# Kernel optimization log

Hardware: AMD Instinct MI355X
Metric: run time of the kernel (lower is better)

The kernel has to match this reference:

```python
import jax, jax.numpy as jnp
import numpy as np

EPS = 1e-5

def _fake_quant(w, axis):
    # symmetric int8 fake-quant with straight-through estimator
    s = jnp.max(jnp.abs(w), axis=axis, keepdims=True) / 127.0 + 1e-8
    q = jnp.clip(jnp.round(w / s), -127.0, 127.0) * s
    return w + jax.lax.stop_gradient(q - w)

def _qconv1x1(x, w, b):
    # x: [B, C_in, Q, H, W]; w: [C_out, C_in] (1x1 kernel); weight fake-quantized
    wq = _fake_quant(w, axis=1)
    return jnp.einsum('bcqhw,oc->boqhw', x, wq) + b[None, :, None, None, None]

def setup_inputs() -> dict:
    key = jax.random.key(0)
    ks = jax.random.split(key, 12)
    B, C, Q, H, W = 8, 256, 4, 40, 40
    x = jax.random.normal(ks[0], (B, C, Q, H, W), dtype=jnp.float32)
    scale = 1.0 / np.sqrt(C)
    Wq = jax.random.normal(ks[1], (C, C), dtype=jnp.float32) * scale
    Wk = jax.random.normal(ks[2], (C, C), dtype=jnp.float32) * scale
    Wv = jax.random.normal(ks[3], (C, C), dtype=jnp.float32) * scale
    Wp = jax.random.normal(ks[4], (C, C), dtype=jnp.float32) * scale
    bq = jnp.zeros((C,), jnp.float32)
    bk = jnp.zeros((C,), jnp.float32)
    bv = jnp.zeros((C,), jnp.float32)
    bp = jnp.zeros((C,), jnp.float32)
    gamma = jnp.ones((C,), jnp.float32)
    beta = jnp.zeros((C,), jnp.float32)
    return {"x": x, "Wq": Wq, "bq": bq, "Wk": Wk, "bk": bk,
            "Wv": Wv, "bv": bv, "Wp": Wp, "bp": bp,
            "gamma": gamma, "beta": beta}

def reference(x, Wq, bq, Wk, bk, Wv, bv, Wp, bp, gamma, beta):
    B, C, Q, H, W = x.shape
    q = _qconv1x1(x, Wq, bq)
    k = _qconv1x1(x, Wk, bk)
    v = _qconv1x1(x, Wv, bv)
    # per-rotation channel attention: [B, Q=4, C, H*W]
    qh = q.reshape(B, C, Q, H * W).transpose(0, 2, 1, 3)
    kh = k.reshape(B, C, Q, H * W).transpose(0, 2, 1, 3)
    vh = v.reshape(B, C, Q, H * W).transpose(0, 2, 1, 3)
    scale = 1.0 / jnp.sqrt(jnp.float32(C // 4))
    attn = jnp.einsum('bqcn,bqdn->bqcd', qh, kh) * scale  # [B,4,C,C]
    attn = jax.nn.softmax(attn, axis=-1)
    out = jnp.einsum('bqcd,bqdn->bqcn', attn, vh)  # [B,4,C,HW]
    out = out.transpose(0, 2, 1, 3).reshape(B, C, Q, H, W)
    out = _qconv1x1(out, Wp, bp)
    # IQBN: per-channel batchnorm with int8 fake-quantized gamma
    mean = jnp.mean(out, axis=(0, 2, 3, 4), keepdims=True)
    var = jnp.var(out, axis=(0, 2, 3, 4), keepdims=True)
    g = _fake_quant(gamma, axis=None)[None, :, None, None, None]
    b = beta[None, :, None, None, None]
    out = (out - mean) * jax.lax.rsqrt(var + EPS) * g + b
    return out
```

## Files before the change

### kernel.cpp

```cpp
#include <hip/hip_runtime.h>
#include <math.h>

#define BB 8
#define CCH 256
#define QQ 4
#define NN 1600
#define BQN 32
#define SP 51200
#define EPSF 1e-5f

typedef __attribute__((ext_vector_type(8))) short bf16x8;
typedef __attribute__((ext_vector_type(4))) float f32x4;

static __device__ inline ushort f2bf(float f) {
  union { float f; unsigned u; } v; v.f = f;
  return (ushort)((v.u + 0x7fffu + ((v.u >> 16) & 1u)) >> 16);
}
static __device__ inline float bf2f(ushort u) {
  union { unsigned u; float f; } v; v.u = ((unsigned)u) << 16;
  return v.f;
}
static __device__ inline void gld16(const ushort* g, ushort* l) {
  __builtin_amdgcn_global_load_lds(
      (const __attribute__((address_space(1))) unsigned int*)g,
      (__attribute__((address_space(3))) unsigned int*)l, 16, 0, 0);
}

__global__ void quant_weights_kernel(const float* Wq, const float* Wk,
                                     const float* Wv, const float* Wp,
                                     const float* gamma,
                                     ushort* wq, ushort* wk, ushort* wvT, ushort* wp,
                                     ushort* wqT, ushort* wkT, ushort* wpT,
                                     float* gq, float* r, float* d2,
                                     float* m_acc, float* v_acc) {
  __shared__ float red[256];
  int blk = blockIdx.x;
  int tid = threadIdx.x;
  if (blk < 1024) {
    int mat = blk >> 8;
    int row = blk & 255;
    const float* W = (mat == 0) ? Wq : (mat == 1) ? Wk : (mat == 2) ? Wv : Wp;
    float w = W[row * 256 + tid];
    red[tid] = fabsf(w);
    __syncthreads();
    for (int s = 128; s > 0; s >>= 1) {
      if (tid < s) red[tid] = fmaxf(red[tid], red[tid + s]);
      __syncthreads();
    }
// ... 2 lines not shown
    ushort qb = f2bf(q);
    if (mat == 0)      { wq[row * 256 + tid] = qb; wqT[tid * 256 + row] = qb; }
    else if (mat == 1) { wk[row * 256 + tid] = qb; wkT[tid * 256 + row] = qb; }
    else if (mat == 2) { wvT[tid * 256 + row] = qb; }
    else               { wp[row * 256 + tid] = qb; wpT[tid * 256 + row] = qb; }
  } else {
    float g = gamma[tid];
    red[tid] = fabsf(g);
    __syncthreads();
    for (int s = 128; s > 0; s >>= 1) {
      if (tid < s) red[tid] = fmaxf(red[tid], red[tid + s]);
      __syncthreads();
    }
    float s = red[0] / 127.0f + 1e-8f;
    gq[tid] = fminf(fmaxf(rintf(g / s), -127.0f), 127.0f) * s;
    for (int i = tid; i < BQN * 256; i += 256) { r[i] = 0.f; d2[i] = 0.f; }
    m_acc[tid] = 0.f;
    v_acc[tid] = 0.f;
  }
}

__global__ __launch_bounds__(256)
void prep_kernel(const float* __restrict__ x, ushort* __restrict__ xb,
                 ushort* __restrict__ xT, float* __restrict__ r) {
  int bqi = blockIdx.z, b = bqi >> 2, q = bqi & 3;
  int s0 = blockIdx.x * 64, c0 = blockIdx.y * 64;
  __shared__ ushort lT[64 * 66];
  int tid = threadIdx.x;
  int c = tid >> 2, nch = (tid & 3) * 16;
  const float* xp = x + ((size_t)(b * CCH + c0 + c) * QQ + q) * NN + s0 + nch;
  union { ushort u[16]; int4 v[2]; } nb;
// ... 17 lines not shown
  *((int4*)xbp + 1) = nb.v[1];
  s += __shfl_down(s, 2);
  s += __shfl_down(s, 1);
  if ((tid & 3) == 0) atomicAdd(&r[bqi * 256 + c0 + c], s);
  __syncthreads();
  int n = tid >> 2, cch = (tid & 3) * 16;
  union { ushort u[16]; int4 v[2]; } o;
#pragma unroll
  for (int i = 0; i < 16; i++) o.u[i] = lT[(cch + i) * 66 + n];
  ushort* dst = xT + (size_t)(bqi * NN + s0 + n) * CCH + c0 + cch;
  *(int4*)dst = o.v[0];
  *((int4*)dst + 1) = o.v[1];
}

__global__ __launch_bounds__(256)
void gram_sym_kernel(const ushort* __restrict__ xb, ushort* __restrict__ Gh,
                     ushort* __restrict__ Gl) {
  __shared__ __align__(16) char smem[16384];
  int t = blockIdx.x, z = blockIdx.y;
  int ty = (t >= 4) + (t >= 7) + (t >= 9);
  int base = ty * 4 - (ty * (ty - 1)) / 2;
  int tx = ty + (t - base);
  int mBase = ty * 64, nBase = tx * 64;
  bool offd = (tx != ty);
  int tid = threadIdx.x, wave = tid >> 6, lane = tid & 63;
  int wm = wave >> 1, wn = wave & 1;
  int col = lane & 15, quad = lane >> 4;
  const ushort* X = xb + (size_t)z * (CCH * NN);
  const ushort* gA = X + (size_t)(mBase + (tid >> 2)) * NN + (tid & 3) * 8;
  const ushort* gB = X + (size_t)(nBase + (tid >> 2)) * NN + (tid & 3) * 8;
  f32x4 acc[2][2];
#pragma unroll
  for (int i = 0; i < 2; i++)
#pragma unroll
    for (int j = 0; j < 2; j++) acc[i][j] = (f32x4){0.f, 0.f, 0.f, 0.f};

  const int nIter = NN / 32;
  gld16(gA, (ushort*)smem + tid * 8);
  gld16(gB, (ushort*)(smem + 4096) + tid * 8);
  for (int it = 0; it < nIter; ++it) {
    int cur = it & 1;
    __syncthreads();
    if (it + 1 < nIter) {
      int kt = (it + 1) << 5;
      char* bb = smem + (cur ^ 1) * 8192;
      gld16(gA + kt, (ushort*)bb + tid * 8);
      gld16(gB + kt, (ushort*)(bb + 4096) + tid * 8);
    }
    const ushort* lA = (const ushort*)(smem + cur * 8192);
    const ushort* lB = lA + 2048;
    bf16x8 af[2], bfr[2];
#pragma unroll
    for (int i = 0; i < 2; i++)
      af[i] = *(const bf16x8*)&lA[(wm * 32 + i * 16 + col) * 32 + quad * 8];
#pragma unroll
    for (int j = 0; j < 2; j++)
      bfr[j] = *(const bf16x8*)&lB[(wn * 32 + j * 16 + col) * 32 + quad * 8];
#pragma unroll
    for (int i = 0; i < 2; i++)
#pragma unroll
      for (int j = 0; j < 2; j++)
        acc[i][j] = __builtin_amdgcn_mfma_f32_16x16x32_bf16(af[i], bfr[j], acc[i][j], 0, 0, 0);
  }
  __syncthreads();
  float* lCw = (float*)smem + wave * 576;
#pragma unroll
  for (int i = 0; i < 2; i++) {
#pragma unroll
    for (int j = 0; j < 2; j++)
#pragma unroll
      for (int rg = 0; rg < 4; rg++)
        lCw[(quad * 4 + rg) * 36 + j * 16 + col] = acc[i][j][rg];
    int mrow0 = mBase + wm * 32 + i * 16;
    int nW = nBase + wn * 32;
    int rr = lane >> 2, cc = (lane & 3) * 8;
    union { ushort u[8]; int4 v; } oh, ol;
#pragma unroll
    for (int t8 = 0; t8 < 8; t8++) {
      float vfl = lCw[rr * 36 + cc + t8];
      ushort hh = f2bf(vfl);
// ... 8 lines not shown
      union { ushort u[8]; int4 v; } th, tl;
#pragma unroll
      for (int t8 = 0; t8 < 8; t8++) {
        float vfl = lCw[(mh + t8) * 36 + nn];
        ushort hh = f2bf(vfl);
        th.u[t8] = hh;
        tl.u[t8] = f2bf(vfl - bf2f(hh));
      }
      size_t offT = (size_t)z * 65536 + (size_t)(nW + nn) * 256 + mrow0 + mh;
      *(int4*)(Gh + offT) = th.v;
      *(int4*)(Gl + offT) = tl.v;
    }
  }
}

__global__ __launch_bounds__(256)
void spk_kernel(const ushort* __restrict__ wq, const ushort* __restrict__ Gh,
                const ushort* __restrict__ Gl, const ushort* __restrict__ wk,
                const float* __restrict__ ug, const float* __restrict__ vg,
                const float* __restrict__ bqv, const float* __restrict__ bkv,
                const float* __restrict__ bvv,
                ushort* __restrict__ P, float* __restrict__ pb) {
  __shared__ __align__(16) char smem[103424];
  int z = blockIdx.y, mBase = blockIdx.x * 32;
  int tid = threadIdx.x, wave = tid >> 6, lane = tid & 63;
  int col = lane & 15, quad = lane >> 4;
  int rA = tid >> 2, sub = (tid & 3) * 8;
  const ushort* Ghz = Gh + (size_t)z * 65536;
  const ushort* Glz = Gl + (size_t)z * 65536;
  ushort* M1h_l = (ushort*)(smem + 69632);
  ushort* M1l_l = M1h_l + 8448;

  f32x4 acc[2][4];
#pragma unroll
  for (int i = 0; i < 2; i++)
#pragma unroll
    for (int j = 0; j < 4; j++) acc[i][j] = (f32x4){0.f, 0.f, 0.f, 0.f};

  auto s1_load = [&](int buf, int kt) {
    ushort* L = (ushort*)(smem + buf * 34816);
    if (tid < 128)
      gld16(wq + (size_t)(mBase + rA) * 256 + kt + sub, L + tid * 8);
    ushort* Lh = L + 1024;
    ushort* Ll = L + 9216;
#pragma unroll
    for (int q = 0; q < 4; q++) {
      int n = q * 64 + rA;
      gld16(Ghz + (size_t)n * 256 + kt + sub, Lh + (q * 256 + tid) * 8);
      gld16(Glz + (size_t)n * 256 + kt + sub, Ll + (q * 256 + tid) * 8);
    }
  };
  s1_load(0, 0);
  for (int it = 0; it < 8; ++it) {
    int cur = it & 1;
    __syncthreads();
    if (it + 1 < 8) s1_load(cur ^ 1, (it + 1) * 32);
    const ushort* L = (const ushort*)(smem + cur * 34816);
    const ushort* lA = L;
    const ushort* lBh = L + 1024;
    const ushort* lBl = L + 9216;
    bf16x8 af[2], bh[4], bl[4];
#pragma unroll
    for (int i = 0; i < 2; i++)
      af[i] = *(const bf16x8*)&lA[(i * 16 + col) * 32 + quad * 8];
#pragma unroll
    for (int j = 0; j < 4; j++) {
      bh[j] = *(const bf16x8*)&lBh[(wave * 64 + j * 16 + col) * 32 + quad * 8];
      bl[j] = *(const bf16x8*)&lBl[(wave * 64 + j * 16 + col) * 32 + quad * 8];
    }
#pragma unroll
    for (int i = 0; i < 2; i++)
#pragma unroll
      for (int j = 0; j < 4; j++) {
        acc[i][j] = __builtin_amdgcn_mfma_f32_16x16x32_bf16(af[i], bh[j], acc[i][j], 0, 0, 0);
        acc[i][j] = __builtin_amdgcn_mfma_f32_16x16x32_bf16(af[i], bl[j], acc[i][j], 0, 0, 0);
      }
  }
#pragma unroll
  for (int i = 0; i < 2; i++)
#pragma unroll
    for (int j = 0; j < 4; j++)
#pragma unroll
      for (int rg = 0; rg < 4; rg++) {
        int ml = i * 16 + quad * 4 + rg;
        int cg = wave * 64 + j * 16 + col;
        float vfl = acc[i][j][rg];
        ushort hh = f2bf(vfl);
        M1h_l[ml * 264 + cg] = hh;
        M1l_l[ml * 264 + cg] = f2bf(vfl - bf2f(hh));
      }

  f32x4 acc2[2][4];
#pragma unroll
  for (int i = 0; i < 2; i++)
#pragma unroll
    for (int j = 0; j < 4; j++) acc2[i][j] = (f32x4){0.f, 0.f, 0.f, 0.f};
  auto s2_load = [&](int buf, int kt) {
    ushort* L = (ushort*)(smem + buf * 34816);
#pragma unroll
    for (int q = 0; q < 4; q++)
      gld16(wk + (size_t)(q * 64 + rA) * 256 + kt + sub, L + (q * 256 + tid) * 8);
  };
  s2_load(0, 0);
  for (int it = 0; it < 8; ++it) {
    int cur = it & 1;
    __syncthreads();
    if (it + 1 < 8) s2_load(cur ^ 1, (it + 1) * 32);
    const ushort* lB = (const ushort*)(smem + cur * 34816);
    int kt = it * 32;
    bf16x8 ah[2], al[2], bfr[4];
#pragma unroll
    for (int i = 0; i < 2; i++) {
      ah[i] = *(const bf16x8*)&M1h_l[(i * 16 + col) * 264 + kt + quad * 8];
      al[i] = *(const bf16x8*)&M1l_l[(i * 16 + col) * 264 + kt + quad * 8];
    }
#pragma unroll
    for (int j = 0; j < 4; j++)
      bfr[j] = *(const bf16x8*)&lB[(wave * 64 + j * 16 + col) * 32 + quad * 8];
#pragma unroll
    for (int i = 0; i < 2; i++)
#pragma unroll
      for (int j = 0; j < 4; j++) {
        acc2[i][j] = __builtin_amdgcn_mfma_f32_16x16x32_bf16(ah[i], bfr[j], acc2[i][j], 0, 0, 0);
        acc2[i][j] = __builtin_amdgcn_mfma_f32_16x16x32_bf16(al[i], bfr[j], acc2[i][j], 0, 0, 0);
      }
  }
  __syncthreads();

  float* Sb = (float*)(smem + 69632);
  float bkc[4], vvc[4];
#pragma unroll
  for (int j = 0; j < 4; j++) {
    int cg = wave * 64 + j * 16 + col;
    bkc[j] = bkv[cg];
    vvc[j] = vg[z * 256 + cg];
  }
#pragma unroll
  for (int i = 0; i < 2; i++)
#pragma unroll
    for (int rg = 0; rg < 4; rg++) {
      int ml = i * 16 + quad * 4 + rg;
      int rglob = mBase + ml;
      float uu = ug[z * 256 + rglob];
      float bqc = bqv[rglob];
#pragma unroll
      for (int j = 0; j < 4; j++)
        Sb[ml * 260 + wave * 64 + j * 16 + col] =
            0.125f * (acc2[i][j][rg] + uu * bkc[j] + bqc * vvc[j] + 1600.0f * bqc * bkc[j]);
    }
  __syncthreads();

  float4 bv4 = *(const float4*)(bvv + lane * 4);
#pragma unroll
  for (int rr8 = 0; rr8 < 8; ++rr8) {
    int rloc = wave * 8 + rr8;
    f32x4 sv = *(const f32x4*)&Sb[rloc * 260 + lane * 4];
    float x0 = sv[0], x1 = sv[1], x2 = sv[2], x3 = sv[3];
    float m = fmaxf(fmaxf(x0, x1), fmaxf(x2, x3));
#pragma unroll
    for (int s = 32; s > 0; s >>= 1) m = fmaxf(m, __shfl_xor(m, s));
    float e0 = expf(x0 - m), e1 = expf(x1 - m), e2 = expf(x2 - m), e3 = expf(x3 - m);
    float t = e0 + e1 + e2 + e3;
#pragma unroll
    for (int s = 32; s > 0; s >>= 1) t += __shfl_xor(t, s);
    float is = 1.0f / t;
    float p0 = e0 * is, p1 = e1 * is, p2 = e2 * is, p3 = e3 * is;
    union { ushort u[4]; uint2 v; } o;
    o.u[0] = f2bf(p0); o.u[1] = f2bf(p1); o.u[2] = f2bf(p2); o.u[3] = f2bf(p3);
    *(uint2*)(P + (size_t)z * 65536 + (size_t)(mBase + rloc) * 256 + lane * 4) = o.v;
    float d = p0 * bv4.x + p1 * bv4.y + p2 * bv4.z + p3 * bv4.w;
#pragma unroll
    for (int s = 32; s > 0; s >>= 1) d += __shfl_xor(d, s);
    if (lane == 0) pb[z * 256 + mBase + rloc] = d;
  }
}

__global__ __launch_bounds__(256)
void pt_kernel(const ushort* __restrict__ P, const ushort* __restrict__ wvT,
               const ushort* __restrict__ wp,
               ushort* __restrict__ Tm, ushort* __restrict__ TmT) {
  __shared__ __align__(16) char smem[53760];
  int z = blockIdx.y, cs = blockIdx.x * 32;
  int tid = threadIdx.x, wave = tid >> 6, lane = tid & 63;
  int col = lane & 15, quad = lane >> 4;
  int rA = tid >> 2, sub = (tid & 3) * 8;
  const ushort* Pz = P + (size_t)z * 65536;
  ushort* N1b = (ushort*)(smem + 36864);

  f32x4 acc[4][2];
#pragma unroll
  for (int i = 0; i < 4; i++)
#pragma unroll
    for (int j = 0; j < 2; j++) acc[i][j] = (f32x4){0.f, 0.f, 0.f, 0.f};
  auto s3_load = [&](int buf, int kt) {
    ushort* L = (ushort*)(smem + buf * 18432);
#pragma unroll
    for (int q = 0; q < 4; q++)
      gld16(Pz + (size_t)(q * 64 + rA) * 256 + kt + sub, L + (q * 256 + tid) * 8);
    if (tid < 128)
      gld16(wvT + (size_t)(cs + rA) * 256 + kt + sub, L + 8192 + tid * 8);
  };
  s3_load(0, 0);
  for (int it = 0; it < 8; ++it) {
    int cur = it & 1;
    __syncthreads();
    if (it + 1 < 8) s3_load(cur ^ 1, (it + 1) * 32);
    const ushort* lP = (const ushort*)(smem + cur * 18432);
    const ushort* lV = lP + 8192;
    bf16x8 af[4], bfr[2];
#pragma unroll
    for (int i = 0; i < 4; i++)
      af[i] = *(const bf16x8*)&lP[(wave * 64 + i * 16 + col) * 32 + quad * 8];
#pragma unroll
    for (int j = 0; j < 2; j++)
      bfr[j] = *(const bf16x8*)&lV[(j * 16 + col) * 32 + quad * 8];
#pragma unroll
    for (int i = 0; i < 4; i++)
#pragma unroll
      for (int j = 0; j < 2; j++)
        acc[i][j] = __builtin_amdgcn_mfma_f32_16x16x32_bf16(af[i], bfr[j], acc[i][j], 0, 0, 0);
  }
#pragma unroll
  for (int i = 0; i < 4; i++)
#pragma unroll
    for (int j = 0; j < 2; j++)
#pragma unroll
      for (int rg = 0; rg < 4; rg++) {
        int e = wave * 64 + i * 16 + quad * 4 + rg;
        int cl = j * 16 + col;
        N1b[cl * 264 + e] = f2bf(acc[i][j][rg]);
      }

  f32x4 acc2[4][2];
#pragma unroll
  for (int i = 0; i < 4; i++)
#pragma unroll
    for (int j = 0; j < 2; j++) acc2[i][j] = (f32x4){0.f, 0.f, 0.f, 0.f};
  auto s4_load = [&](int buf, int kt) {
    ushort* L = (ushort*)(smem + buf * 18432);
#pragma unroll
    for (int q = 0; q < 4; q++)
      gld16(wp + (size_t)(q * 64 + rA) * 256 + kt + sub, L + (q * 256 + tid) * 8);
  };
  s4_load(0, 0);
  for (int it = 0; it < 8; ++it) {
    int cur = it & 1;
    __syncthreads();
    if (it + 1 < 8) s4_load(cur ^ 1, (it + 1) * 32);
    const ushort* lW = (const ushort*)(smem + cur * 18432);
    int kt = it * 32;
    bf16x8 af[4], bfr[2];
#pragma unroll
    for (int i = 0; i < 4; i++)
      af[i] = *(const bf16x8*)&lW[(wave * 64 + i * 16 + col) * 32 + quad * 8];
#pragma unroll
    for (int j = 0; j < 2; j++)
      bfr[j] = *(const bf16x8*)&N1b[(j * 16 + col) * 264 + kt + quad * 8];
#pragma unroll
    for (int i = 0; i < 4; i++)
#pragma unroll
      for (int j = 0; j < 2; j++)
        acc2[i][j] = __builtin_amdgcn_mfma_f32_16x16x32_bf16(af[i], bfr[j], acc2[i][j], 0, 0, 0);
  }
  __syncthreads();
  float* lCw = (float*)smem + wave * 576;
#pragma unroll
  for (int i = 0; i < 4; i++) {
#pragma unroll
    for (int j = 0; j < 2; j++)
#pragma unroll
      for (int rg = 0; rg < 4; rg++)
        lCw[(quad * 4 + rg) * 36 + j * 16 + col] = acc2[i][j][rg];
    int oW = wave * 64 + i * 16;
    int rr = lane >> 2, cc = (lane & 3) * 8;
    union { ushort u[8]; int4 v; } o;
#pragma unroll
    for (int t8 = 0; t8 < 8; t8++) o.u[t8] = f2bf(lCw[rr * 36 + cc + t8]);
    *(int4*)(Tm + (size_t)z * 65536 + (size_t)(oW + rr) * 256 + cs + cc) = o.v;
    int nn = lane >> 1, mh = (lane & 1) * 8;
    union { ushort u[8]; int4 v; } o2;
#pragma unroll
    for (int t8 = 0; t8 < 8; t8++) o2.u[t8] = f2bf(lCw[(mh + t8) * 36 + nn]);
    *(int4*)(TmT + (size_t)z * 65536 + (size_t)(cs + nn) * 256 + oW + mh) = o2.v;
  }
}

template<int MODE>
__global__ __launch_bounds__(256)
void gemm64(const ushort* __restrict__ A, long sA, const ushort* __restrict__ A2,
            const ushort* __restrict__ B, long sB, const ushort* __restrict__ B2,
            void* __restrict__ C1, void* __restrict__ C2, long sC) {
  constexpr bool SPB = (MODE == 0 || MODE == 4);
  constexpr bool SPA = (MODE == 1);
  constexpr int BUFB = (SPA || SPB) ? 12288 : 8192;
  __shared__ __align__(16) char smem[2 * BUFB];
  int z = blockIdx.z;
  int mBase = blockIdx.y * 64, nBase = blockIdx.x * 64;
  int tid = threadIdx.x, wave = tid >> 6, lane = tid & 63;
  int wm = wave >> 1, wn = wave & 1;
  int col = lane & 15, quad = lane >> 4;
  const ushort* gA = A + (size_t)z * sA + (size_t)(mBase + (tid >> 2)) * 256 + (tid & 3) * 8;
  const ushort* gB = B + (size_t)z * sB + (size_t)(nBase + (tid >> 2)) * 256 + (tid & 3) * 8;
  const ushort* gX = nullptr;
  if (SPB) gX = B2 + (size_t)z * sB + (size_t)(nBase + (tid >> 2)) * 256 + (tid & 3) * 8;
  if (SPA) gX = A2 + (size_t)z * sA + (size_t)(mBase + (tid >> 2)) * 256 + (tid & 3) * 8;

  f32x4 acc[2][2];
#pragma unroll
  for (int i = 0; i < 2; i++)
#pragma unroll
    for (int j = 0; j < 2; j++) acc[i][j] = (f32x4){0.f, 0.f, 0.f, 0.f};

  {
    char* bb = smem;
    gld16(gA, (ushort*)bb + tid * 8);
    gld16(gB, (ushort*)(bb + 4096) + tid * 8);
    if (SPA || SPB) gld16(gX, (ushort*)(bb + 8192) + tid * 8);
  }
  for (int it = 0; it < 8; ++it) {
    int cur = it & 1;
    __syncthreads();
    if (it + 1 < 8) {
      int kt = (it + 1) * 32;
      char* bb = smem + (cur ^ 1) * BUFB;
      gld16(gA + kt, (ushort*)bb + tid * 8);
      gld16(gB + kt, (ushort*)(bb + 4096) + tid * 8);
      if (SPA || SPB) gld16(gX + kt, (ushort*)(bb + 8192) + tid * 8);
    }
    const ushort* lA = (const ushort*)(smem + cur * BUFB);
    const ushort* lB = lA + 2048;
    const ushort* lX = lA + 4096;
    bf16x8 af[2], bfv[2], xf[2];
#pragma unroll
    for (int i = 0; i < 2; i++)
      af[i] = *(const bf16x8*)&lA[(wm * 32 + i * 16 + col) * 32 + quad * 8];
#pragma unroll
    for (int j = 0; j < 2; j++)
      bfv[j] = *(const bf16x8*)&lB[(wn * 32 + j * 16 + col) * 32 + quad * 8];
    if (SPB) {
#pragma unroll
      for (int j = 0; j < 2; j++)
        xf[j] = *(const bf16x8*)&lX[(wn * 32 + j * 16 + col) * 32 + quad * 8];
    } else if (SPA) {
#pragma unroll
      for (int i = 0; i < 2; i++)
        xf[i] = *(const bf16x8*)&lX[(wm * 32 + i * 16 + col) * 32 + quad * 8];
    }
#pragma unroll
    for (int i = 0; i < 2; i++)
#pragma unroll
      for (int j = 0; j < 2; j++) {
        acc[i][j] = __builtin_amdgcn_mfma_f32_16x16x32_bf16(af[i], bfv[j], acc[i][j], 0, 0, 0);
        if (SPB)
          acc[i][j] = __builtin_amdgcn_mfma_f32_16x16x32_bf16(af[i], xf[j], acc[i][j], 0, 0, 0);
        if (SPA)
          acc[i][j] = __builtin_amdgcn_mfma_f32_16x16x32_bf16(xf[i], bfv[j], acc[i][j], 0, 0, 0);
      }
  }

  if (MODE == 4) {
    const ushort* Tz = A + (size_t)z * sA;
    float* d2 = (float*)C1;
#pragma unroll
    for (int i = 0; i < 2; i++) {
      int mr = mBase + wm * 32 + i * 16 + quad * 4;
#pragma unroll
      for (int rg = 0; rg < 4; rg++) {
        float p = 0.f;
#pragma unroll
        for (int j = 0; j < 2; j++)
          p += acc[i][j][rg] * bf2f(Tz[(mr + rg) * 256 + nBase + wn * 32 + j * 16 + col]);
        p += __shfl_down(p, 8);
        p += __shfl_down(p, 4);
        p += __shfl_down(p, 2);
        p += __shfl_down(p, 1);
        if (col == 0) atomicAdd(d2 + z * 256 + mr + rg, p);
      }
    }
    return;
  }
}

__global__ __launch_bounds__(256)
void uv_kernel(const ushort* __restrict__ wqT, const ushort* __restrict__ wkT,
               const float* __restrict__ r, float* __restrict__ u,
               float* __restrict__ vv) {
  int bq = blockIdx.x, sel = blockIdx.y, c = threadIdx.x;
  __shared__ float rs[256];
  rs[c] = r[bq * 256 + c];
  __syncthreads();
  const ushort* WT = sel ? wkT : wqT;
  float s = 0.f;
  for (int i = 0; i < 256; i++) s += bf2f(WT[i * 256 + c]) * rs[i];
  (sel ? vv : u)[bq * 256 + c] = s;
}

__global__ __launch_bounds__(256)
void bo_d1_kernel(const ushort* __restrict__ wpT, const ushort* __restrict__ TmT,
                  const float* __restrict__ pb, const float* __restrict__ rb,
                  const float* __restrict__ bp, const float* __restrict__ d2,
                  float* __restrict__ bo, float* __restrict__ m_acc,
                  float* __restrict__ v_acc) {
  int z = blockIdx.x, o = threadIdx.x;
  __shared__ float sp[256], sr[256];
  sp[o] = pb[z * 256 + o];
  sr[o] = rb[z * 256 + o];
  __syncthreads();
  float bv = bp[o], d1 = 0.f;
  const ushort* Tz = TmT + (size_t)z * 65536;
  for (int c = 0; c < 256; c++) {
    bv += bf2f(wpT[c * 256 + o]) * sp[c];
    d1 += bf2f(Tz[c * 256 + o]) * sr[c];
  }
  bo[z * 256 + o] = bv;
  atomicAdd(m_acc + o, d1 + 1600.0f * bv);
  atomicAdd(v_acc + o, d2[z * 256 + o] + 2.0f * bv * d1 + 1600.0f * bv * bv);
}

__global__ __launch_bounds__(256)
void final_kernel(const ushort* __restrict__ Tm, const ushort* __restrict__ xT,
                  const float* __restrict__ bo, const float* __restrict__ m_acc,
                  const float* __restrict__ v_acc, const float* __restrict__ gq,
                  const float* __restrict__ beta, float* __restrict__ out) {
  __shared__ __align__(16) char smem[32768];
  float* lC = (float*)smem;
  int z = blockIdx.z;
  int mBase = blockIdx.y * 128, nBase = blockIdx.x * 128;
  int tid = threadIdx.x, wave = tid >> 6, lane = tid & 63;
  int wm = wave >> 1, wn = wave & 1;
  int col = lane & 15, quad = lane >> 4;
  int srow = tid >> 2, skc = (tid & 3) * 8;
// ... 107 lines not shown
  ushort* wqT  = wvT + 65536;
  ushort* wkT  = wqT + 65536;
  ushort* wpT  = wkT + 65536;
  ushort* xb   = wpT + 65536;
  ushort* xT   = xb + (size_t)BQN * CCH * NN;
  ushort* Gh   = xT + (size_t)BQN * CCH * NN;
  ushort* Gl   = Gh + (size_t)BQN * 65536;
  ushort* P    = Gl + (size_t)BQN * 65536;
  ushort* Tm   = P + (size_t)BQN * 65536;
  ushort* TmT  = Tm + (size_t)BQN * 65536;
  float*  r    = (float*)(TmT + (size_t)BQN * 65536);
  float*  u    = r + 8192;
  float*  vv   = u + 8192;
  float*  pb   = vv + 8192;
  float*  bo   = pb + 8192;
  float*  d2   = bo + 8192;
  float*  m_acc = d2 + 8192;
  float*  v_acc = m_acc + 256;
  float*  gq   = v_acc + 256;

  quant_weights_kernel<<<1025, 256, 0, stream>>>(Wq, Wk, Wv, Wp, gamma,
                                                 wq, wk, wvT, wp, wqT, wkT, wpT,
                                                 gq, r, d2, m_acc, v_acc);
  prep_kernel<<<dim3(NN / 64, CCH / 64, BQN), 256, 0, stream>>>(x, xb, xT, r);
  uv_kernel<<<dim3(BQN, 2), 256, 0, stream>>>(wqT, wkT, r, u, vv);
  gram_sym_kernel<<<dim3(10, BQN), 256, 0, stream>>>(xb, Gh, Gl);
  spk_kernel<<<dim3(8, BQN), 256, 0, stream>>>(wq, Gh, Gl, wk, u, vv, bq, bk, bv, P, pb);
  pt_kernel<<<dim3(8, BQN), 256, 0, stream>>>(P, wvT, wp, Tm, TmT);
  gemm64<4><<<dim3(4, 4, BQN), 256, 0, stream>>>(
      Tm, 65536, nullptr, Gh, 65536, Gl, d2, nullptr, 0);
  bo_d1_kernel<<<BQN, 256, 0, stream>>>(wpT, TmT, pb, r, bp, d2, bo, m_acc, v_acc);
  final_kernel<<<dim3(13, 2, BQN), 256, 0, stream>>>(Tm, xT, bo, m_acc, v_acc,
                                                     gq, beta, out);
}
```

Before: 250.9 us.

## Load MFMA operands directly from global, fuse uv into gram, widen spk/pt blocks

Replaces LDS double-buffered global_load_lds staging in the gram, spk, pt and d2 GEMMs with direct per-lane 16-byte global loads feeding MFMA. It folds the uv reduction into an extra block of the gram kernel and moves spk and pt to 512-thread blocks with smaller per-wave tiles and less shared memory. The d2 buffer is dropped and its values are accumulated straight into v_acc. This saves launches, LDS traffic and barriers, but relies on L1/L2 for operand reuse and loses explicit load/compute overlap.

```diff
diff --git a/kernel.cpp b/kernel.cpp
--- a/kernel.cpp
+++ b/kernel.cpp
@@ -20,6 +20,9 @@
   union { unsigned u; float f; } v; v.u = ((unsigned)u) << 16;
   return v.f;
 }
+static __device__ inline bf16x8 ldg8(const ushort* p) {
+  return *(const bf16x8*)p;
+}
 static __device__ inline void gld16(const ushort* g, ushort* l) {
   __builtin_amdgcn_global_load_lds(
       (const __attribute__((address_space(1))) unsigned int*)g,
@@ -31,7 +34,7 @@
                                      const float* gamma,
                                      ushort* wq, ushort* wk, ushort* wvT, ushort* wp,
                                      ushort* wqT, ushort* wkT, ushort* wpT,
-                                     float* gq, float* r, float* d2,
+                                     float* gq, float* r,
                                      float* m_acc, float* v_acc) {
   __shared__ float red[256];
   int blk = blockIdx.x;
@@ -64,7 +67,7 @@
     }
     float s = red[0] / 127.0f + 1e-8f;
     gq[tid] = fminf(fmaxf(rintf(g / s), -127.0f), 127.0f) * s;
-    for (int i = tid; i < BQN * 256; i += 256) { r[i] = 0.f; d2[i] = 0.f; }
+    for (int i = tid; i < BQN * 256; i += 256) r[i] = 0.f;
     m_acc[tid] = 0.f;
     v_acc[tid] = 0.f;
   }
@@ -112,56 +115,56 @@
 }
 
 __global__ __launch_bounds__(256)
-void gram_sym_kernel(const ushort* __restrict__ xb, ushort* __restrict__ Gh,
-                     ushort* __restrict__ Gl) {
-  __shared__ __align__(16) char smem[16384];
+void gram_uv_kernel(const ushort* __restrict__ xb, ushort* __restrict__ Gh,
+                    ushort* __restrict__ Gl,
+                    const ushort* __restrict__ wqT, const ushort* __restrict__ wkT,
+                    const float* __restrict__ r, float* __restrict__ u,
+                    float* __restrict__ vv) {
+  __shared__ __align__(16) float lCw_s[2304];
+  __shared__ float rs[256];
   int t = blockIdx.x, z = blockIdx.y;
+  int tid = threadIdx.x;
+  if (t == 10) {
+    rs[tid] = r[z * 256 + tid];
+    __syncthreads();
+    float su = 0.f, sv = 0.f;
+    for (int i = 0; i < 256; i++) {
+      float rv = rs[i];
+      su += bf2f(wqT[i * 256 + tid]) * rv;
+      sv += bf2f(wkT[i * 256 + tid]) * rv;
+    }
+    u[z * 256 + tid] = su;
+    vv[z * 256 + tid] = sv;
+    return;
+  }
   int ty = (t >= 4) + (t >= 7) + (t >= 9);
   int base = ty * 4 - (ty * (ty - 1)) / 2;
   int tx = ty + (t - base);
   int mBase = ty * 64, nBase = tx * 64;
   bool offd = (tx != ty);
-  int tid = threadIdx.x, wave = tid >> 6, lane = tid & 63;
+  int wave = tid >> 6, lane = tid & 63;
   int wm = wave >> 1, wn = wave & 1;
   int col = lane & 15, quad = lane >> 4;
   const ushort* X = xb + (size_t)z * (CCH * NN);
-  const ushort* gA = X + (size_t)(mBase + (tid >> 2)) * NN + (tid & 3) * 8;
-  const ushort* gB = X + (size_t)(nBase + (tid >> 2)) * NN + (tid & 3) * 8;
+  const ushort* pA0 = X + (size_t)(mBase + wm * 32 + col) * NN + quad * 8;
+  const ushort* pA1 = pA0 + (size_t)16 * NN;
+  const ushort* pB0 = X + (size_t)(nBase + wn * 32 + col) * NN + quad * 8;
+  const ushort* pB1 = pB0 + (size_t)16 * NN;
   f32x4 acc[2][2];
 #pragma unroll
   for (int i = 0; i < 2; i++)
 #pragma unroll
     for (int j = 0; j < 2; j++) acc[i][j] = (f32x4){0.f, 0.f, 0.f, 0.f};
-
-  const int nIter = NN / 32;
-  gld16(gA, (ushort*)smem + tid * 8);
-  gld16(gB, (ushort*)(smem + 4096) + tid * 8);
-  for (int it = 0; it < nIter; ++it) {
-    int cur = it & 1;
-    __syncthreads();
-    if (it + 1 < nIter) {
-      int kt = (it + 1) << 5;
-      char* bb = smem + (cur ^ 1) * 8192;
-      gld16(gA + kt, (ushort*)bb + tid * 8);
-      gld16(gB + kt, (ushort*)(bb + 4096) + tid * 8);
-    }
-    const ushort* lA = (const ushort*)(smem + cur * 8192);
-    const ushort* lB = lA + 2048;
-    bf16x8 af[2], bfr[2];
-#pragma unroll
-    for (int i = 0; i < 2; i++)
-      af[i] = *(const bf16x8*)&lA[(wm * 32 + i * 16 + col) * 32 + quad * 8];
-#pragma unroll
-    for (int j = 0; j < 2; j++)
-      bfr[j] = *(const bf16x8*)&lB[(wn * 32 + j * 16 + col) * 32 + quad * 8];
-#pragma unroll
-    for (int i = 0; i < 2; i++)
-#pragma unroll
-      for (int j = 0; j < 2; j++)
-        acc[i][j] = __builtin_amdgcn_mfma_f32_16x16x32_bf16(af[i], bfr[j], acc[i][j], 0, 0, 0);
-  }
-  __syncthreads();
-  float* lCw = (float*)smem + wave * 576;
+#pragma unroll 2
+  for (int kk = 0; kk < NN; kk += 32) {
+    bf16x8 a0 = ldg8(pA0 + kk), a1 = ldg8(pA1 + kk);
+    bf16x8 b0 = ldg8(pB0 + kk), b1 = ldg8(pB1 + kk);
+    acc[0][0] = __builtin_amdgcn_mfma_f32_16x16x32_bf16(a0, b0, acc[0][0], 0, 0, 0);
+    acc[0][1] = __builtin_amdgcn_mfma_f32_16x16x32_bf16(a0, b1, acc[0][1], 0, 0, 0);
+    acc[1][0] = __builtin_amdgcn_mfma_f32_16x16x32_bf16(a1, b0, acc[1][0], 0, 0, 0);
+    acc[1][1] = __builtin_amdgcn_mfma_f32_16x16x32_bf16(a1, b1, acc[1][1], 0, 0, 0);
+  }
+  float* lCw = lCw_s + wave * 576;
 #pragma unroll
   for (int i = 0; i < 2; i++) {
 #pragma unroll
@@ -200,124 +203,96 @@
   }
 }
 
-__global__ __launch_bounds__(256)
+__global__ __launch_bounds__(512)
 void spk_kernel(const ushort* __restrict__ wq, const ushort* __restrict__ Gh,
                 const ushort* __restrict__ Gl, const ushort* __restrict__ wk,
                 const float* __restrict__ ug, const float* __restrict__ vg,
                 const float* __restrict__ bqv, const float* __restrict__ bkv,
                 const float* __restrict__ bvv,
                 ushort* __restrict__ P, float* __restrict__ pb) {
-  __shared__ __align__(16) char smem[103424];
+  __shared__ __align__(16) char smem[33792];
+  ushort* M1h_l = (ushort*)smem;
+  ushort* M1l_l = M1h_l + 8448;
   int z = blockIdx.y, mBase = blockIdx.x * 32;
-  int tid = threadIdx.x, wave = tid >> 6, lane = tid & 63;
+  int tid = threadIdx.x, w = tid >> 6, lane = tid & 63;
   int col = lane & 15, quad = lane >> 4;
-  int rA = tid >> 2, sub = (tid & 3) * 8;
   const ushort* Ghz = Gh + (size_t)z * 65536;
   const ushort* Glz = Gl + (size_t)z * 65536;
-  ushort* M1h_l = (ushort*)(smem + 69632);
-  ushort* M1l_l = M1h_l + 8448;
-
-  f32x4 acc[2][4];
-#pragma unroll
-  for (int i = 0; i < 2; i++)
-#pragma unroll
-    for (int j = 0; j < 4; j++) acc[i][j] = (f32x4){0.f, 0.f, 0.f, 0.f};
-
-  auto s1_load = [&](int buf, int kt) {
-    ushort* L = (ushort*)(smem + buf * 34816);
-    if (tid < 128)
-      gld16(wq + (size_t)(mBase + rA) * 256 + kt + sub, L + tid * 8);
-    ushort* Lh = L + 1024;
-    ushort* Ll = L + 9216;
-#pragma unroll
-    for (int q = 0; q < 4; q++) {
-      int n = q * 64 + rA;
-      gld16(Ghz + (size_t)n * 256 + kt + sub, Lh + (q * 256 + tid) * 8);
-      gld16(Glz + (size_t)n * 256 + kt + sub, Ll + (q * 256 + tid) * 8);
-    }
-  };
-  s1_load(0, 0);
-  for (int it = 0; it < 8; ++it) {
-    int cur = it & 1;
-    __syncthreads();
-    if (it + 1 < 8) s1_load(cur ^ 1, (it + 1) * 32);
-    const ushort* L = (const ushort*)(smem + cur * 34816);
-    const ushort* lA = L;
-    const ushort* lBh = L + 1024;
-    const ushort* lBl = L + 9216;
-    bf16x8 af[2], bh[4], bl[4];
-#pragma unroll
-    for (int i = 0; i < 2; i++)
-      af[i] = *(const bf16x8*)&lA[(i * 16 + col) * 32 + quad * 8];
-#pragma unroll
-    for (int j = 0; j < 4; j++) {
-      bh[j] = *(const bf16x8*)&lBh[(wave * 64 + j * 16 + col) * 32 + quad * 8];
-      bl[j] = *(const bf16x8*)&lBl[(wave * 64 + j * 16 + col) * 32 + quad * 8];
-    }
-#pragma unroll
-    for (int i = 0; i < 2; i++)
-#pragma unroll
-      for (int j = 0; j < 4; j++) {
-        acc[i][j] = __builtin_amdgcn_mfma_f32_16x16x32_bf16(af[i], bh[j], acc[i][j], 0, 0, 0);
-        acc[i][j] = __builtin_amdgcn_mfma_f32_16x16x32_bf16(af[i], bl[j], acc[i][j], 0, 0, 0);
-      }
-  }
-#pragma unroll
-  for (int i = 0; i < 2; i++)
-#pragma unroll
-    for (int j = 0; j < 4; j++)
+
+  f32x4 acc[2][2];
+#pragma unroll
+  for (int i = 0; i < 2; i++)
+#pragma unroll
+    for (int j = 0; j < 2; j++) acc[i][j] = (f32x4){0.f, 0.f, 0.f, 0.f};
+  {
+    const ushort* pA0 = wq + (size_t)(mBase + col) * 256 + quad * 8;
+    const ushort* pA1 = pA0 + 16 * 256;
+    const ushort* pH0 = Ghz + (size_t)(w * 32 + col) * 256 + quad * 8;
+    const ushort* pH1 = pH0 + 16 * 256;
+    const ushort* pL0 = Glz + (size_t)(w * 32 + col) * 256 + quad * 8;
+    const ushort* pL1 = pL0 + 16 * 256;
+#pragma unroll
+    for (int kk = 0; kk < 256; kk += 32) {
+      bf16x8 a0 = ldg8(pA0 + kk), a1 = ldg8(pA1 + kk);
+      bf16x8 h0 = ldg8(pH0 + kk), h1 = ldg8(pH1 + kk);
+      bf16x8 l0 = ldg8(pL0 + kk), l1 = ldg8(pL1 + kk);
+      acc[0][0] = __builtin_amdgcn_mfma_f32_16x16x32_bf16(a0, h0, acc[0][0], 0, 0, 0);
+      acc[0][0] = __builtin_amdgcn_mfma_f32_16x16x32_bf16(a0, l0, acc[0][0], 0, 0, 0);
+      acc[0][1] = __builtin_amdgcn_mfma_f32_16x16x32_bf16(a0, h1, acc[0][1], 0, 0, 0);
+      acc[0][1] = __builtin_amdgcn_mfma_f32_16x16x32_bf16(a0, l1, acc[0][1], 0, 0, 0);
+      acc[1][0] = __builtin_amdgcn_mfma_f32_16x16x32_bf16(a1, h0, acc[1][0], 0, 0, 0);
+      acc[1][0] = __builtin_amdgcn_mfma_f32_16x16x32_bf16(a1, l0, acc[1][0], 0, 0, 0);
+      acc[1][1] = __builtin_amdgcn_mfma_f32_16x16x32_bf16(a1, h1, acc[1][1], 0, 0, 0);
+      acc[1][1] = __builtin_amdgcn_mfma_f32_16x16x32_bf16(a1, l1, acc[1][1], 0, 0, 0);
+    }
+  }
+#pragma unroll
+  for (int i = 0; i < 2; i++)
+#pragma unroll
+    for (int j = 0; j < 2; j++)
 #pragma unroll
       for (int rg = 0; rg < 4; rg++) {
         int ml = i * 16 + quad * 4 + rg;
-        int cg = wave * 64 + j * 16 + col;
+        int cg = w * 32 + j * 16 + col;
         float vfl = acc[i][j][rg];
         ushort hh = f2bf(vfl);
         M1h_l[ml * 264 + cg] = hh;
         M1l_l[ml * 264 + cg] = f2bf(vfl - bf2f(hh));
       }
-
-  f32x4 acc2[2][4];
-#pragma unroll
-  for (int i = 0; i < 2; i++)
-#pragma unroll
-    for (int j = 0; j < 4; j++) acc2[i][j] = (f32x4){0.f, 0.f, 0.f, 0.f};
-  auto s2_load = [&](int buf, int kt) {
-    ushort* L = (ushort*)(smem + buf * 34816);
-#pragma unroll
-    for (int q = 0; q < 4; q++)
-      gld16(wk + (size_t)(q * 64 + rA) * 256 + kt + sub, L + (q * 256 + tid) * 8);
-  };
-  s2_load(0, 0);
-  for (int it = 0; it < 8; ++it) {
-    int cur = it & 1;
-    __syncthreads();
-    if (it + 1 < 8) s2_load(cur ^ 1, (it + 1) * 32);
-    const ushort* lB = (const ushort*)(smem + cur * 34816);
-    int kt = it * 32;
-    bf16x8 ah[2], al[2], bfr[4];
-#pragma unroll
-    for (int i = 0; i < 2; i++) {
-      ah[i] = *(const bf16x8*)&M1h_l[(i * 16 + col) * 264 + kt + quad * 8];
-      al[i] = *(const bf16x8*)&M1l_l[(i * 16 + col) * 264 + kt + quad * 8];
-    }
-#pragma unroll
-    for (int j = 0; j < 4; j++)
-      bfr[j] = *(const bf16x8*)&lB[(wave * 64 + j * 16 + col) * 32 + quad * 8];
-#pragma unroll
-    for (int i = 0; i < 2; i++)
-#pragma unroll
-      for (int j = 0; j < 4; j++) {
-        acc2[i][j] = __builtin_amdgcn_mfma_f32_16x16x32_bf16(ah[i], bfr[j], acc2[i][j], 0, 0, 0);
-        acc2[i][j] = __builtin_amdgcn_mfma_f32_16x16x32_bf16(al[i], bfr[j], acc2[i][j], 0, 0, 0);
-      }
-  }
-  __syncthreads();
-
-  float* Sb = (float*)(smem + 69632);
-  float bkc[4], vvc[4];
-#pragma unroll
-  for (int j = 0; j < 4; j++) {
-    int cg = wave * 64 + j * 16 + col;
+  __syncthreads();
+
+  f32x4 acc2[2][2];
+#pragma unroll
+  for (int i = 0; i < 2; i++)
+#pragma unroll
+    for (int j = 0; j < 2; j++) acc2[i][j] = (f32x4){0.f, 0.f, 0.f, 0.f};
+  {
+    const ushort* pW0 = wk + (size_t)(w * 32 + col) * 256 + quad * 8;
+    const ushort* pW1 = pW0 + 16 * 256;
+#pragma unroll
+    for (int kk = 0; kk < 256; kk += 32) {
+      bf16x8 ah0 = *(const bf16x8*)&M1h_l[(col) * 264 + kk + quad * 8];
+      bf16x8 ah1 = *(const bf16x8*)&M1h_l[(16 + col) * 264 + kk + quad * 8];
+      bf16x8 al0 = *(const bf16x8*)&M1l_l[(col) * 264 + kk + quad * 8];
+      bf16x8 al1 = *(const bf16x8*)&M1l_l[(16 + col) * 264 + kk + quad * 8];
+      bf16x8 b0 = ldg8(pW0 + kk), b1 = ldg8(pW1 + kk);
+      acc2[0][0] = __builtin_amdgcn_mfma_f32_16x16x32_bf16(ah0, b0, acc2[0][0], 0, 0, 0);
+      acc2[0][0] = __builtin_amdgcn_mfma_f32_16x16x32_bf16(al0, b0, acc2[0][0], 0, 0, 0);
+      acc2[0][1] = __builtin_amdgcn_mfma_f32_16x16x32_bf16(ah0, b1, acc2[0][1], 0, 0, 0);
+      acc2[0][1] = __builtin_amdgcn_mfma_f32_16x16x32_bf16(al0, b1, acc2[0][1], 0, 0, 0);
+      acc2[1][0] = __builtin_amdgcn_mfma_f32_16x16x32_bf16(ah1, b0, acc2[1][0], 0, 0, 0);
+      acc2[1][0] = __builtin_amdgcn_mfma_f32_16x16x32_bf16(al1, b0, acc2[1][0], 0, 0, 0);
+      acc2[1][1] = __builtin_amdgcn_mfma_f32_16x16x32_bf16(ah1, b1, acc2[1][1], 0, 0, 0);
+      acc2[1][1] = __builtin_amdgcn_mfma_f32_16x16x32_bf16(al1, b1, acc2[1][1], 0, 0, 0);
+    }
+  }
+  __syncthreads();
+
+  float* Sb = (float*)smem;
+  float bkc[2], vvc[2];
+#pragma unroll
+  for (int j = 0; j < 2; j++) {
+    int cg = w * 32 + j * 16 + col;
     bkc[j] = bkv[cg];
     vvc[j] = vg[z * 256 + cg];
   }
@@ -330,16 +305,16 @@
       float uu = ug[z * 256 + rglob];
       float bqc = bqv[rglob];
 #pragma unroll
-      for (int j = 0; j < 4; j++)
-        Sb[ml * 260 + wave * 64 + j * 16 + col] =
+      for (int j = 0; j < 2; j++)
+        Sb[ml * 260 + w * 32 + j * 16 + col] =
             0.125f * (acc2[i][j][rg] + uu * bkc[j] + bqc * vvc[j] + 1600.0f * bqc * bkc[j]);
     }
   __syncthreads();
 
   float4 bv4 = *(const float4*)(bvv + lane * 4);
 #pragma unroll
-  for (int rr8 = 0; rr8 < 8; ++rr8) {
-    int rloc = wave * 8 + rr8;
+  for (int rr4 = 0; rr4 < 4; ++rr4) {
+    int rloc = w * 4 + rr4;
     f32x4 sv = *(const f32x4*)&Sb[rloc * 260 + lane * 4];
     float x0 = sv[0], x1 = sv[1], x2 = sv[2], x3 = sv[3];
     float m = fmaxf(fmaxf(x0, x1), fmaxf(x2, x3));
@@ -361,103 +336,79 @@
   }
 }
 
-__global__ __launch_bounds__(256)
+__global__ __launch_bounds__(512)
 void pt_kernel(const ushort* __restrict__ P, const ushort* __restrict__ wvT,
                const ushort* __restrict__ wp,
                ushort* __restrict__ Tm, ushort* __restrict__ TmT) {
-  __shared__ __align__(16) char smem[53760];
+  __shared__ __align__(16) char smem[18432];
+  ushort* N1b = (ushort*)smem;
   int z = blockIdx.y, cs = blockIdx.x * 32;
-  int tid = threadIdx.x, wave = tid >> 6, lane = tid & 63;
+  int tid = threadIdx.x, w = tid >> 6, lane = tid & 63;
   int col = lane & 15, quad = lane >> 4;
-  int rA = tid >> 2, sub = (tid & 3) * 8;
   const ushort* Pz = P + (size_t)z * 65536;
-  ushort* N1b = (ushort*)(smem + 36864);
-
-  f32x4 acc[4][2];
-#pragma unroll
-  for (int i = 0; i < 4; i++)
+
+  f32x4 acc[2][2];
+#pragma unroll
+  for (int i = 0; i < 2; i++)
 #pragma unroll
     for (int j = 0; j < 2; j++) acc[i][j] = (f32x4){0.f, 0.f, 0.f, 0.f};
-  auto s3_load = [&](int buf, int kt) {
-    ushort* L = (ushort*)(smem + buf * 18432);
-#pragma unroll
-    for (int q = 0; q < 4; q++)
-      gld16(Pz + (size_t)(q * 64 + rA) * 256 + kt + sub, L + (q * 256 + tid) * 8);
-    if (tid < 128)
-      gld16(wvT + (size_t)(cs + rA) * 256 + kt + sub, L + 8192 + tid * 8);
-  };
-  s3_load(0, 0);
-  for (int it = 0; it < 8; ++it) {
-    int cur = it & 1;
-    __syncthreads();
-    if (it + 1 < 8) s3_load(cur ^ 1, (it + 1) * 32);
-    const ushort* lP = (const ushort*)(smem + cur * 18432);
-    const ushort* lV = lP + 8192;
-    bf16x8 af[4], bfr[2];
-#pragma unroll
-    for (int i = 0; i < 4; i++)
-      af[i] = *(const bf16x8*)&lP[(wave * 64 + i * 16 + col) * 32 + quad * 8];
+  {
+    const ushort* pP0 = Pz + (size_t)(w * 32 + col) * 256 + quad * 8;
+    const ushort* pP1 = pP0 + 16 * 256;
+    const ushort* pV0 = wvT + (size_t)(cs + col) * 256 + quad * 8;
+    const ushort* pV1 = pV0 + 16 * 256;
+#pragma unroll
+    for (int kk = 0; kk < 256; kk += 32) {
+      bf16x8 a0 = ldg8(pP0 + kk), a1 = ldg8(pP1 + kk);
+      bf16x8 b0 = ldg8(pV0 + kk), b1 = ldg8(pV1 + kk);
+      acc[0][0] = __builtin_amdgcn_mfma_f32_16x16x32_bf16(a0, b0, acc[0][0], 0, 0, 0);
+      acc[0][1] = __builtin_amdgcn_mfma_f32_16x16x32_bf16(a0, b1, acc[0][1], 0, 0, 0);
+      acc[1][0] = __builtin_amdgcn_mfma_f32_16x16x32_bf16(a1, b0, acc[1][0], 0, 0, 0);
+      acc[1][1] = __builtin_amdgcn_mfma_f32_16x16x32_bf16(a1, b1, acc[1][1], 0, 0, 0);
+    }
+  }
+#pragma unroll
+  for (int i = 0; i < 2; i++)
 #pragma unroll
     for (int j = 0; j < 2; j++)
-      bfr[j] = *(const bf16x8*)&lV[(j * 16 + col) * 32 + quad * 8];
-#pragma unroll
-    for (int i = 0; i < 4; i++)
-#pragma unroll
-      for (int j = 0; j < 2; j++)
-        acc[i][j] = __builtin_amdgcn_mfma_f32_16x16x32_bf16(af[i], bfr[j], acc[i][j], 0, 0, 0);
-  }
-#pragma unroll
-  for (int i = 0; i < 4; i++)
-#pragma unroll
-    for (int j = 0; j < 2; j++)
 #pragma unroll
       for (int rg = 0; rg < 4; rg++) {
-        int e = wave * 64 + i * 16 + quad * 4 + rg;
+        int e = w * 32 + i * 16 + quad * 4 + rg;
         int cl = j * 16 + col;
         N1b[cl * 264 + e] = f2bf(acc[i][j][rg]);
       }
-
-  f32x4 acc2[4][2];
-#pragma unroll
-  for (int i = 0; i < 4; i++)
+  __syncthreads();
+
+  f32x4 acc2[2][2];
+#pragma unroll
+  for (int i = 0; i < 2; i++)
 #pragma unroll
     for (int j = 0; j < 2; j++) acc2[i][j] = (f32x4){0.f, 0.f, 0.f, 0.f};
-  auto s4_load = [&](int buf, int kt) {
-    ushort* L = (ushort*)(smem + buf * 18432);
-#pragma unroll
-    for (int q = 0; q < 4; q++)
-      gld16(wp + (size_t)(q * 64 + rA) * 256 + kt + sub, L + (q * 256 + tid) * 8);
-  };
-  s4_load(0, 0);
-  for (int it = 0; it < 8; ++it) {
-    int cur = it & 1;
-    __syncthreads();
-    if (it + 1 < 8) s4_load(cur ^ 1, (it + 1) * 32);
-    const ushort* lW = (const ushort*)(smem + cur * 18432);
-    int kt = it * 32;
-    bf16x8 af[4], bfr[2];
-#pragma unroll
-    for (int i = 0; i < 4; i++)
-      af[i] = *(const bf16x8*)&lW[(wave * 64 + i * 16 + col) * 32 + quad * 8];
-#pragma unroll
-    for (int j = 0; j < 2; j++)
-      bfr[j] = *(const bf16x8*)&N1b[(j * 16 + col) * 264 + kt + quad * 8];
-#pragma unroll
-    for (int i = 0; i < 4; i++)
-#pragma unroll
-      for (int j = 0; j < 2; j++)
-        acc2[i][j] = __builtin_amdgcn_mfma_f32_16x16x32_bf16(af[i], bfr[j], acc2[i][j], 0, 0, 0);
-  }
-  __syncthreads();
-  float* lCw = (float*)smem + wave * 576;
-#pragma unroll
-  for (int i = 0; i < 4; i++) {
+  {
+    const ushort* pW0 = wp + (size_t)(w * 32 + col) * 256 + quad * 8;
+    const ushort* pW1 = pW0 + 16 * 256;
+#pragma unroll
+    for (int kk = 0; kk < 256; kk += 32) {
+      bf16x8 a0 = ldg8(pW0 + kk), a1 = ldg8(pW1 + kk);
+      bf16x8 b0 = *(const bf16x8*)&N1b[(col) * 264 + kk + quad * 8];
+      bf16x8 b1 = *(const bf16x8*)&N1b[(16 + col) * 264 + kk + quad * 8];
+      acc2[0][0] = __builtin_amdgcn_mfma_f32_16x16x32_bf16(a0, b0, acc2[0][0], 0, 0, 0);
+      acc2[0][1] = __builtin_amdgcn_mfma_f32_16x16x32_bf16(a0, b1, acc2[0][1], 0, 0, 0);
+      acc2[1][0] = __builtin_amdgcn_mfma_f32_16x16x32_bf16(a1, b0, acc2[1][0], 0, 0, 0);
+      acc2[1][1] = __builtin_amdgcn_mfma_f32_16x16x32_bf16(a1, b1, acc2[1][1], 0, 0, 0);
+    }
+  }
+  __syncthreads();
+
+  float* lCw = (float*)smem + w * 576;
+#pragma unroll
+  for (int i = 0; i < 2; i++) {
 #pragma unroll
     for (int j = 0; j < 2; j++)
 #pragma unroll
       for (int rg = 0; rg < 4; rg++)
         lCw[(quad * 4 + rg) * 36 + j * 16 + col] = acc2[i][j][rg];
-    int oW = wave * 64 + i * 16;
+    int oW = w * 32 + i * 16;
     int rr = lane >> 2, cc = (lane & 3) * 8;
     union { ushort u[8]; int4 v; } o;
 #pragma unroll
@@ -471,120 +422,64 @@
   }
 }
 
-template<int MODE>
 __global__ __launch_bounds__(256)
-void gemm64(const ushort* __restrict__ A, long sA, const ushort* __restrict__ A2,
-            const ushort* __restrict__ B, long sB, const ushort* __restrict__ B2,
-            void* __restrict__ C1, void* __restrict__ C2, long sC) {
-  constexpr bool SPB = (MODE == 0 || MODE == 4);
-  constexpr bool SPA = (MODE == 1);
-  constexpr int BUFB = (SPA || SPB) ? 12288 : 8192;
-  __shared__ __align__(16) char smem[2 * BUFB];
+void dsq_kernel(const ushort* __restrict__ Tm, const ushort* __restrict__ Gh,
+                const ushort* __restrict__ Gl, float* __restrict__ v_acc) {
   int z = blockIdx.z;
   int mBase = blockIdx.y * 64, nBase = blockIdx.x * 64;
   int tid = threadIdx.x, wave = tid >> 6, lane = tid & 63;
   int wm = wave >> 1, wn = wave & 1;
   int col = lane & 15, quad = lane >> 4;
-  const ushort* gA = A + (size_t)z * sA + (size_t)(mBase + (tid >> 2)) * 256 + (tid & 3) * 8;
-  const ushort* gB = B + (size_t)z * sB + (size_t)(nBase + (tid >> 2)) * 256 + (tid & 3) * 8;
-  const ushort* gX = nullptr;
-  if (SPB) gX = B2 + (size_t)z * sB + (size_t)(nBase + (tid >> 2)) * 256 + (tid & 3) * 8;
-  if (SPA) gX = A2 + (size_t)z * sA + (size_t)(mBase + (tid >> 2)) * 256 + (tid & 3) * 8;
-
+  const ushort* Tz = Tm + (size_t)z * 65536;
+  const ushort* Ghz = Gh + (size_t)z * 65536;
+  const ushort* Glz = Gl + (size_t)z * 65536;
+  const ushort* pA0 = Tz + (size_t)(mBase + wm * 32 + col) * 256 + quad * 8;
+  const ushort* pA1 = pA0 + 16 * 256;
+  const ushort* pH0 = Ghz + (size_t)(nBase + wn * 32 + col) * 256 + quad * 8;
+  const ushort* pH1 = pH0 + 16 * 256;
+  const ushort* pL0 = Glz + (size_t)(nBase + wn * 32 + col) * 256 + quad * 8;
+  const ushort* pL1 = pL0 + 16 * 256;
   f32x4 acc[2][2];
 #pragma unroll
   for (int i = 0; i < 2; i++)
 #pragma unroll
     for (int j = 0; j < 2; j++) acc[i][j] = (f32x4){0.f, 0.f, 0.f, 0.f};
-
-  {
-    char* bb = smem;
-    gld16(gA, (ushort*)bb + tid * 8);
-    gld16(gB, (ushort*)(bb + 4096) + tid * 8);
-    if (SPA || SPB) gld16(gX, (ushort*)(bb + 8192) + tid * 8);
-  }
-  for (int it = 0; it < 8; ++it) {
-    int cur = it & 1;
-    __syncthreads();
-    if (it + 1 < 8) {
-      int kt = (it + 1) * 32;
-      char* bb = smem + (cur ^ 1) * BUFB;
-      gld16(gA + kt, (ushort*)bb + tid * 8);
-      gld16(gB + kt, (ushort*)(bb + 4096) + tid * 8);
-      if (SPA || SPB) gld16(gX + kt, (ushort*)(bb + 8192) + tid * 8);
-    }
-    const ushort* lA = (const ushort*)(smem + cur * BUFB);
-    const ushort* lB = lA + 2048;
-    const ushort* lX = lA + 4096;
-    bf16x8 af[2], bfv[2], xf[2];
-#pragma unroll
-    for (int i = 0; i < 2; i++)
-      af[i] = *(const bf16x8*)&lA[(wm * 32 + i * 16 + col) * 32 + quad * 8];
-#pragma unroll
-    for (int j = 0; j < 2; j++)
-      bfv[j] = *(const bf16x8*)&lB[(wn * 32 + j * 16 + col) * 32 + quad * 8];
-    if (SPB) {
+#pragma unroll
+  for (int kk = 0; kk < 256; kk += 32) {
+    bf16x8 a0 = ldg8(pA0 + kk), a1 = ldg8(pA1 + kk);
+    bf16x8 h0 = ldg8(pH0 + kk), h1 = ldg8(pH1 + kk);
+    bf16x8 l0 = ldg8(pL0 + kk), l1 = ldg8(pL1 + kk);
+    acc[0][0] = __builtin_amdgcn_mfma_f32_16x16x32_bf16(a0, h0, acc[0][0], 0, 0, 0);
+    acc[0][0] = __builtin_amdgcn_mfma_f32_16x16x32_bf16(a0, l0, acc[0][0], 0, 0, 0);
+    acc[0][1] = __builtin_amdgcn_mfma_f32_16x16x32_bf16(a0, h1, acc[0][1], 0, 0, 0);
+    acc[0][1] = __builtin_amdgcn_mfma_f32_16x16x32_bf16(a0, l1, acc[0][1], 0, 0, 0);
+    acc[1][0] = __builtin_amdgcn_mfma_f32_16x16x32_bf16(a1, h0, acc[1][0], 0, 0, 0);
+    acc[1][0] = __builtin_amdgcn_mfma_f32_16x16x32_bf16(a1, l0, acc[1][0], 0, 0, 0);
+    acc[1][1] = __builtin_amdgcn_mfma_f32_16x16x32_bf16(a1, h1, acc[1][1], 0, 0, 0);
+    acc[1][1] = __builtin_amdgcn_mfma_f32_16x16x32_bf16(a1, l1, acc[1][1], 0, 0, 0);
+  }
+#pragma unroll
+  for (int i = 0; i < 2; i++) {
+    int mr = mBase + wm * 32 + i * 16 + quad * 4;
+#pragma unroll
+    for (int rg = 0; rg < 4; rg++) {
+      float p = 0.f;
 #pragma unroll
       for (int j = 0; j < 2; j++)
-        xf[j] = *(const bf16x8*)&lX[(wn * 32 + j * 16 + col) * 32 + quad * 8];
-    } else if (SPA) {
-#pragma unroll
-      for (int i = 0; i < 2; i++)
-        xf[i] = *(const bf16x8*)&lX[(wm * 32 + i * 16 + col) * 32 + quad * 8];
-    }
-#pragma unroll
-    for (int i = 0; i < 2; i++)
-#pragma unroll
-      for (int j = 0; j < 2; j++) {
-        acc[i][j] = __builtin_amdgcn_mfma_f32_16x16x32_bf16(af[i], bfv[j], acc[i][j], 0, 0, 0);
-        if (SPB)
-          acc[i][j] = __builtin_amdgcn_mfma_f32_16x16x32_bf16(af[i], xf[j], acc[i][j], 0, 0, 0);
-        if (SPA)
-          acc[i][j] = __builtin_amdgcn_mfma_f32_16x16x32_bf16(xf[i], bfv[j], acc[i][j], 0, 0, 0);
-      }
-  }
-
-  if (MODE == 4) {
-    const ushort* Tz = A + (size_t)z * sA;
-    float* d2 = (float*)C1;
-#pragma unroll
-    for (int i = 0; i < 2; i++) {
-      int mr = mBase + wm * 32 + i * 16 + quad * 4;
-#pragma unroll
-      for (int rg = 0; rg < 4; rg++) {
-        float p = 0.f;
-#pragma unroll
-        for (int j = 0; j < 2; j++)
-          p += acc[i][j][rg] * bf2f(Tz[(mr + rg) * 256 + nBase + wn * 32 + j * 16 + col]);
-        p += __shfl_down(p, 8);
-        p += __shfl_down(p, 4);
-        p += __shfl_down(p, 2);
-        p += __shfl_down(p, 1);
-        if (col == 0) atomicAdd(d2 + z * 256 + mr + rg, p);
-      }
-    }
-    return;
-  }
-}
-
-__global__ __launch_bounds__(256)
-void uv_kernel(const ushort* __restrict__ wqT, const ushort* __restrict__ wkT,
-               const float* __restrict__ r, float* __restrict__ u,
-               float* __restrict__ vv) {
-  int bq = blockIdx.x, sel = blockIdx.y, c = threadIdx.x;
-  __shared__ float rs[256];
-  rs[c] = r[bq * 256 + c];
-  __syncthreads();
-  const ushort* WT = sel ? wkT : wqT;
-  float s = 0.f;
-  for (int i = 0; i < 256; i++) s += bf2f(WT[i * 256 + c]) * rs[i];
-  (sel ? vv : u)[bq * 256 + c] = s;
+        p += acc[i][j][rg] * bf2f(Tz[(mr + rg) * 256 + nBase + wn * 32 + j * 16 + col]);
+      p += __shfl_down(p, 8);
+      p += __shfl_down(p, 4);
+      p += __shfl_down(p, 2);
+      p += __shfl_down(p, 1);
+      if (col == 0) atomicAdd(v_acc + mr + rg, p);
+    }
+  }
 }
 
 __global__ __launch_bounds__(256)
 void bo_d1_kernel(const ushort* __restrict__ wpT, const ushort* __restrict__ TmT,
                   const float* __restrict__ pb, const float* __restrict__ rb,
-                  const float* __restrict__ bp, const float* __restrict__ d2,
+                  const float* __restrict__ bp,
                   float* __restrict__ bo, float* __restrict__ m_acc,
                   float* __restrict__ v_acc) {
   int z = blockIdx.x, o = threadIdx.x;
@@ -600,7 +495,7 @@
   }
   bo[z * 256 + o] = bv;
   atomicAdd(m_acc + o, d1 + 1600.0f * bv);
-  atomicAdd(v_acc + o, d2[z * 256 + o] + 2.0f * bv * d1 + 1600.0f * bv * bv);
+  atomicAdd(v_acc + o, 2.0f * bv * d1 + 1600.0f * bv * bv);
 }
 
 __global__ __launch_bounds__(256)
@@ -738,22 +633,19 @@
   float*  vv   = u + 8192;
   float*  pb   = vv + 8192;
   float*  bo   = pb + 8192;
-  float*  d2   = bo + 8192;
-  float*  m_acc = d2 + 8192;
+  float*  m_acc = bo + 8192;
   float*  v_acc = m_acc + 256;
   float*  gq   = v_acc + 256;
 
   quant_weights_kernel<<<1025, 256, 0, stream>>>(Wq, Wk, Wv, Wp, gamma,
                                                  wq, wk, wvT, wp, wqT, wkT, wpT,
-                                                 gq, r, d2, m_acc, v_acc);
+                                                 gq, r, m_acc, v_acc);
   prep_kernel<<<dim3(NN / 64, CCH / 64, BQN), 256, 0, stream>>>(x, xb, xT, r);
-  uv_kernel<<<dim3(BQN, 2), 256, 0, stream>>>(wqT, wkT, r, u, vv);
-  gram_sym_kernel<<<dim3(10, BQN), 256, 0, stream>>>(xb, Gh, Gl);
-  spk_kernel<<<dim3(8, BQN), 256, 0, stream>>>(wq, Gh, Gl, wk, u, vv, bq, bk, bv, P, pb);
-  pt_kernel<<<dim3(8, BQN), 256, 0, stream>>>(P, wvT, wp, Tm, TmT);
-  gemm64<4><<<dim3(4, 4, BQN), 256, 0, stream>>>(
-      Tm, 65536, nullptr, Gh, 65536, Gl, d2, nullptr, 0);
-  bo_d1_kernel<<<BQN, 256, 0, stream>>>(wpT, TmT, pb, r, bp, d2, bo, m_acc, v_acc);
+  gram_uv_kernel<<<dim3(11, BQN), 256, 0, stream>>>(xb, Gh, Gl, wqT, wkT, r, u, vv);
+  spk_kernel<<<dim3(8, BQN), 512, 0, stream>>>(wq, Gh, Gl, wk, u, vv, bq, bk, bv, P, pb);
+  pt_kernel<<<dim3(8, BQN), 512, 0, stream>>>(P, wvT, wp, Tm, TmT);
+  dsq_kernel<<<dim3(4, 4, BQN), 256, 0, stream>>>(Tm, Gh, Gl, v_acc);
+  bo_d1_kernel<<<BQN, 256, 0, stream>>>(wpT, TmT, pb, r, bp, bo, m_acc, v_acc);
   final_kernel<<<dim3(13, 2, BQN), 256, 0, stream>>>(Tm, xT, bo, m_acc, v_acc,
                                                      gq, beta, out);
 }
```

After: 293.9 us. +17.1%, slower.
